# Performance work log

Measured on AMD Instinct MI355X. Metric: run time of the kernel, lower is better.

## Reference

```python
import jax, jax.numpy as jnp
import numpy as np

B, LD, LQ = 32, 512, 32
E, NF = 300, 4
D = E + NF            # doc_input_size = 304
M = 16                # fofe_max_length == max_len
ALPHA = 0.9
VOCAB = 50000
H = 256
SAMPLE_NUM = 256
POS_N = 128           # int(sample_num * (1 - neg_ratio))
NEG_N = SAMPLE_NUM - POS_N
R = min(M, LD - 2)    # candidate negative lengths = 16
PPL = NEG_N // R + 1  # negatives drawn per length = 9


def setup_inputs() -> dict:
    key = jax.random.key(0)
    ks = jax.random.split(key, 16)
    emb = jax.random.normal(ks[0], (VOCAB, E), jnp.float32) * 0.1
    emb = emb.at[0].set(0.0)  # padding_idx=0
    doc = jax.random.randint(ks[1], (B, LD), 1, VOCAB)
    doc_f = jax.random.normal(ks[2], (B, LD, NF), jnp.float32) * 0.1
    query = jax.random.randint(ks[3], (B, LQ), 1, VOCAB)
    target_s = jax.random.randint(ks[4], (B,), 1, LD - M - 2)
    span = jax.random.randint(ks[5], (B,), 0, M)  # ans_span = target_e - target_s < fofe_max_length
    target_e = target_s + span
    rand_length = jax.random.permutation(ks[6], R)  # torch.randperm(min(max_len, L-2))
    # rand_position[i] ~ randint(1, LD - rand_length[i] - 1)
    u = jax.random.uniform(ks[7], (R, PPL))
    size = (LD - rand_length - 2).astype(jnp.float32)[:, None]
    rand_position = 1 + jnp.floor(u * size).astype(jnp.int32)
    rand_idx = jax.random.randint(ks[8], (NEG_N,), 0, B)  # faithful to original (dim-0 size used as bound)
    perm_idx = jax.random.permutation(ks[9], SAMPLE_NUM)

    def w(k, o, i):
        return jax.random.normal(k, (o, i), jnp.float32) * (1.0 / np.sqrt(i))

    CIN = 3 * D + E  # 1212
    W1 = w(ks[10], 4 * H, CIN)
    W2 = w(ks[11], 4 * H, 4 * H)
    W3 = w(ks[12], 4 * H, 4 * H)
    W4 = w(ks[13], 2 * H, 4 * H)
    W5 = w(ks[14], 1, 2 * H)
    doc_mask = jnp.zeros((B, LD), bool)
    query_mask = jnp.zeros((B, LQ), bool)
    return dict(doc=doc, doc_f=doc_f, query=query, target_s=target_s, target_e=target_e,
                doc_mask=doc_mask, query_mask=query_mask, emb=emb,
                W1=W1, W2=W2, W3=W3, W4=W4, W5=W5,
                rand_length=rand_length, rand_position=rand_position,
                rand_idx=rand_idx, perm_idx=perm_idx)


def _fofe_codes(x):
    """x: [B, D, LD] -> forward/inverse FOFE codes [B, D, M, LD].
    fwd[b,c,l,t] = sum_{k=0}^{l} alpha^k x[b,c,t-k]; inv mirrors to the right."""
    fwd_terms = jnp.stack(
        [(ALPHA ** k) * jnp.pad(x, ((0, 0), (0, 0), (k, 0)))[..., :LD] for k in range(M)], axis=2)
    inv_terms = jnp.stack(
        [(ALPHA ** k) * jnp.pad(x, ((0, 0), (0, 0), (0, k)))[..., k:] for k in range(M)], axis=2)
    return jnp.cumsum(fwd_terms, axis=2), jnp.cumsum(inv_terms, axis=2)


def _cnn(x, W1, W2, W3, W4, W5):
    h = jax.nn.relu(jnp.einsum('oi,bis->bos', W1, x))
    h = jax.nn.relu(jnp.einsum('oi,bis->bos', W2, h))
    h = jax.nn.relu(jnp.einsum('oi,bis->bos', W3, h))
    h = jax.nn.relu(jnp.einsum('oi,bis->bos', W4, h))
    return jax.nn.sigmoid(jnp.einsum('oi,bis->bos', W5, h))


def reference(doc, doc_f, query, target_s, target_e, doc_mask, query_mask, emb,
              W1, W2, W3, W4, W5, rand_length, rand_position, rand_idx, perm_idx):
    # input_embedding (dropout_emb = 0, pos/ner disabled)
    doc_input = jnp.concatenate([emb[doc], doc_f], axis=-1)  # [B, LD, D]
    x = jnp.swapaxes(doc_input, 1, 2)                         # [B, D, LD]
    fwd, inv = _fofe_codes(x)                                 # [B, D, M, LD] each

    # --- positive samples: gold span + left/right full contexts ---
    b = jnp.arange(B)
    span = target_e - target_s
    ans = fwd[b, :, span, target_e]                               # [B, D]
    l_ctx = fwd[b, :, M - 1, jnp.maximum(target_s - 1, 0)]        # [B, D]
    r_ctx = inv[b, :, M - 1, jnp.minimum(target_e + 1, LD - 1)]   # [B, D]
    pos = jnp.concatenate([l_ctx, ans, r_ctx], axis=-1)          # [B, 3D]
    pos = jnp.broadcast_to(pos[:, :, None], (B, 3 * D, POS_N))

    # --- negative samples: random spans of each length in rand_length ---
    rl = rand_length[:, None]                                     # [R, 1]
    neg_ans = fwd[:, :, rl, rand_position].reshape(B, D, R * PPL)
    neg_l = fwd[:, :, M - 1, rand_position - 1].reshape(B, D, R * PPL)
    neg_r = inv[:, :, M - 1, rand_position + rl + 1].reshape(B, D, R * PPL)
    rand_cat = jnp.concatenate([neg_l, neg_ans, neg_r], axis=1)   # [B, 3D, R*PPL]
    neg = rand_cat[:, :, rand_idx]                                # [B, 3D, NEG_N]

    # --- shuffle pos+neg, build query FOFE, run cnn, mse (sum) loss ---
    ctx_ans = jnp.concatenate([pos, neg], axis=-1)[:, :, perm_idx]
    target = jnp.concatenate(
        [jnp.ones((B, 1, POS_N), jnp.float32), jnp.zeros((B, 1, NEG_N), jnp.float32)],
        axis=-1)[:, :, perm_idx]
    qw = ALPHA ** jnp.arange(LQ - 1, -1, -1, dtype=jnp.float32)   # fofe_linear weights
    qf = jnp.einsum('t,bte->be', qw, emb[query])                  # [B, E]
    qb = jnp.broadcast_to(qf[:, :, None], (B, E, SAMPLE_NUM))
    dq_input = jnp.concatenate([ctx_ans, qb], axis=1)             # [B, 3D+E, S]
    score = _cnn(dq_input, W1, W2, W3, W4, W5)                    # [B, 1, S]
    loss = jnp.sum((score - target) ** 2)                         # mse_loss(size_average=False)
    return loss
```

## Files before the change

### kernel.cpp

```cpp
#include <hip/hip_runtime.h>
#include <hip/hip_bf16.h>

#define B_    32
#define LD_   512
#define LQ_   32
#define E_    300
#define NF_   4
#define D_    304
#define M_    16
#define ALPHA_ 0.9f
#define CIN_  1212
#define KP1_  1280
#define NCOL_ 1056
#define NPAD_ 1088
#define PPL_  9
#define NEG_N_ 128

typedef short short8 __attribute__((ext_vector_type(8)));
typedef float f32x4 __attribute__((ext_vector_type(4)));

__device__ __forceinline__ unsigned short f2bf(float f) {
    unsigned int x = __float_as_uint(f);
    unsigned int r = (x + 0x7FFFu + ((x >> 16) & 1u)) >> 16;
    return (unsigned short)r;
}

__global__ __launch_bounds__(320) void prep(
    const int* __restrict__ doc, const float* __restrict__ doc_f,
    const int* __restrict__ query,
    const int* __restrict__ target_s, const int* __restrict__ target_e,
    const float* __restrict__ emb,
    const int* __restrict__ rand_length, const int* __restrict__ rand_position,
    const float* __restrict__ W1, const float* __restrict__ W2,
    const float* __restrict__ W3, const float* __restrict__ W4,
    unsigned short* __restrict__ W1b, unsigned short* __restrict__ W2b,
    unsigned short* __restrict__ W3b, unsigned short* __restrict__ W4b,
    unsigned short* __restrict__ Ft, float* __restrict__ zbuf,
    unsigned* __restrict__ done)
{
    int bid = blockIdx.x;
    int tid = threadIdx.x;

    if (bid < NCOL_) {
        int b = bid / 33;
        int col = bid % 33;
        __shared__ int   s_t[3][16];
        __shared__ float s_w[3][16];
        __shared__ int   s_row[3][16];
        if (tid < 48) {
            int part = tid >> 4, k = tid & 15;
            int t; float valid;
            if (col == 0) {
                int ts = target_s[b], te = target_e[b];
                int span = te - ts;
                if (part == 0)      { t = ts - 1 - k;  valid = (t >= 0) ? 1.f : 0.f; }
                else if (part == 1) { t = te - k;      valid = (k <= span && t >= 0) ? 1.f : 0.f; }
                else                { t = te + 1 + k;  valid = (t < LD_) ? 1.f : 0.f; }
            } else {
                int j = col - 1;
                int r = j / PPL_, p = j - r * PPL_;
                int rl = rand_length[r];
                int rp = rand_position[r * PPL_ + p];
                if (part == 0)      { t = rp - 1 - k;      valid = (t >= 0) ? 1.f : 0.f; }
                else if (part == 1) { t = rp - k;          valid = (k <= rl && t >= 0) ? 1.f : 0.f; }
                else                { t = rp + rl + 1 + k; valid = (t < LD_) ? 1.f : 0.f; }
            }
            float w = (valid != 0.f) ? powf(ALPHA_, (float)k) : 0.f;
            t = min(max(t, 0), LD_ - 1);
            s_t[part][k] = t;
            s_w[part][k] = w;
            s_row[part][k] = doc[b * LD_ + t];
        }
        __syncthreads();

        unsigned short* out = Ft + (size_t)bid * KP1_;
        int g = tid;
        if (g < 228) {
            int part = g / 76;
            int g2 = g - part * 76;
            int cc = g2 * 4;
            float ax = 0.f, ay = 0.f, az = 0.f, aw = 0.f;
            if (cc < 300) {
                for (int i = 0; i < 16; ++i) {
                    float4 v = *(const float4*)(emb + (size_t)s_row[part][i] * E_ + cc);
                    float wv = s_w[part][i];
                    ax += wv * v.x; ay += wv * v.y; az += wv * v.z; aw += wv * v.w;
                }
            } else {
                for (int i = 0; i < 16; ++i) {
                    float4 v = *(const float4*)(doc_f + ((size_t)b * LD_ + s_t[part][i]) * NF_);
                    float wv = s_w[part][i];
                    ax += wv * v.x; ay += wv * v.y; az += wv * v.z; aw += wv * v.w;
                }
            }
            ushort4 o; o.x = f2bf(ax); o.y = f2bf(ay); o.z = f2bf(az); o.w = f2bf(aw);
            *(ushort4*)(out + 4 * g) = o;
        } else if (g < 303) {
            int ce = (g - 228) * 4;
            float ax = 0.f, ay = 0.f, az = 0.f, aw = 0.f;
            float wv = powf(ALPHA_, (float)(LQ_ - 1));
            for (int i = 0; i < 32; ++i) {
                int row = query[b * LQ_ + i];
                float4 v = *(const float4*)(emb + (size_t)row * E_ + ce);
                ax += wv * v.x; ay += wv * v.y; az += wv * v.z; aw += wv * v.w;
                wv *= (1.0f / ALPHA_);
            }
            ushort4 o; o.x = f2bf(ax); o.y = f2bf(ay); o.z = f2bf(az); o.w = f2bf(aw);
            *(ushort4*)(out + 4 * g) = o;
        } else {
            ushort4 z; z.x = 0; z.y = 0; z.z = 0; z.w = 0;
            *(ushort4*)(out + 4 * g) = z;
        }
    } else if (bid < 2000) {
        const long n1 = 1024L * 320;
        const long n2 = 1024L * 1024L / 4;
        const long n4 = 512L * 1024L / 4;
        const long total = n1 + 2 * n2 + n4;
        long stride = 944L * 320L;
        for (long i = (long)(bid - NCOL_) * 320L + tid; i < total; i += stride) {
            ushort4 o;
            if (i < n1) {
                long m = i / 320; int k4 = (int)(i - m * 320);
                if (k4 < 303) {
                    float4 v = *(const float4*)(W1 + m * CIN_ + k4 * 4);
                    o.x = f2bf(v.x); o.y = f2bf(v.y); o.z = f2bf(v.z); o.w = f2bf(v.w);
                } else { o.x = 0; o.y = 0; o.z = 0; o.w = 0; }
                *(ushort4*)(W1b + i * 4) = o;
            } else if (i < n1 + n2) {
                long j = i - n1;
                float4 v = *(const float4*)(W2 + j * 4);
                o.x = f2bf(v.x); o.y = f2bf(v.y); o.z = f2bf(v.z); o.w = f2bf(v.w);
                *(ushort4*)(W2b + j * 4) = o;
            } else if (i < n1 + 2 * n2) {
                long j = i - n1 - n2;
                float4 v = *(const float4*)(W3 + j * 4);
                o.x = f2bf(v.x); o.y = f2bf(v.y); o.z = f2bf(v.z); o.w = f2bf(v.w);
                *(ushort4*)(W3b + j * 4) = o;
            } else {
                long j = i - n1 - 2 * n2;
                float4 v = *(const float4*)(W4 + j * 4);
                o.x = f2bf(v.x); o.y = f2bf(v.y); o.z = f2bf(v.z); o.w = f2bf(v.w);
                *(ushort4*)(W4b + j * 4) = o;
            }
        }
    } else if (bid < 2032) {
        int row = NCOL_ + (bid - 2000);
        ushort4 z; z.x = 0; z.y = 0; z.z = 0; z.w = 0;
        *(ushort4*)(Ft + (size_t)row * KP1_ + tid * 4) = z;
    } else {
        for (int i = tid; i < NPAD_; i += 320) zbuf[i] = 0.f;
        if (tid == 0) *done = 0u;
    }
}

struct GemmS { unsigned short A[2][64][72]; unsigned short B[2][64][72]; };

__device__ __forceinline__ void gemm_core(
    const unsigned short* __restrict__ A,
    const unsigned short* __restrict__ Bm,
    int K, int m0, int n0, GemmS& sh, f32x4 acc[4])
{
    int tid = threadIdx.x;
    int w = tid >> 6, lane = tid & 63;
    int wm = (w >> 1) * 32, wn = (w & 1) * 32;
    int lr = tid >> 2;
    int ls = (tid & 3) * 16;
    int fr = lane & 15, fk = (lane >> 4) * 8;

    const unsigned short* Arow = A + (size_t)(m0 + lr) * K + ls;
    const unsigned short* Brow = Bm + (size_t)(n0 + lr) * K + ls;

    #pragma unroll
    for (int t = 0; t < 4; ++t) { acc[t][0]=0.f; acc[t][1]=0.f; acc[t][2]=0.f; acc[t][3]=0.f; }

    int nk = K >> 6;
    *(uint4*)&sh.A[0][lr][ls]     = *(const uint4*)(Arow);
    *(uint4*)&sh.A[0][lr][ls + 8] = *(const uint4*)(Arow + 8);
    *(uint4*)&sh.B[0][lr][ls]     = *(const uint4*)(Brow);
    *(uint4*)&sh.B[0][lr][ls + 8] = *(const uint4*)(Brow + 8);
    __syncthreads();
    int cur = 0;
    for (int i = 0; i < nk; ++i) {
        uint4 na0, na1, nb0, nb1;
        bool more = (i + 1 < nk);
        if (more) {
            const unsigned short* An = Arow + (size_t)(i + 1) * 64;
            const unsigned short* Bn = Brow + (size_t)(i + 1) * 64;
            na0 = *(const uint4*)(An);
            na1 = *(const uint4*)(An + 8);
            nb0 = *(const uint4*)(Bn);
            nb1 = *(const uint4*)(Bn + 8);
        }
        #pragma unroll
        for (int s = 0; s < 2; ++s) {
            short8 fa0 = *(const short8*)&sh.A[cur][wm + fr][s * 32 + fk];
            short8 fa1 = *(const short8*)&sh.A[cur][wm + 16 + fr][s * 32 + fk];
            short8 fb0 = *(const short8*)&sh.B[cur][wn + fr][s * 32 + fk];
            short8 fb1 = *(const short8*)&sh.B[cur][wn + 16 + fr][s * 32 + fk];
            acc[0] = __builtin_amdgcn_mfma_f32_16x16x32_bf16(fa0, fb0, acc[0], 0, 0, 0);
            acc[1] = __builtin_amdgcn_mfma_f32_16x16x32_bf16(fa0, fb1, acc[1], 0, 0, 0);
            acc[2] = __builtin_amdgcn_mfma_f32_16x16x32_bf16(fa1, fb0, acc[2], 0, 0, 0);
            acc[3] = __builtin_amdgcn_mfma_f32_16x16x32_bf16(fa1, fb1, acc[3], 0, 0, 0);
        }
        if (more) {
            int nb = cur ^ 1;
            *(uint4*)&sh.A[nb][lr][ls]     = na0;
            *(uint4*)&sh.A[nb][lr][ls + 8] = na1;
            *(uint4*)&sh.B[nb][lr][ls]     = nb0;
            *(uint4*)&sh.B[nb][lr][ls + 8] = nb1;
        }
        __syncthreads();
        cur ^= 1;
    }
}

__global__ __launch_bounds__(256) void gemm_relu(
    const unsigned short* __restrict__ A,
    const unsigned short* __restrict__ Bm,
    unsigned short* __restrict__ C, int M, int K)
{
    __shared__ GemmS sh;
    int m0 = blockIdx.x * 64, n0 = blockIdx.y * 64;
    f32x4 acc[4];
    gemm_core(A, Bm, K, m0, n0, sh, acc);
    int tid = threadIdx.x;
    int w = tid >> 6, lane = tid & 63;
    int wm = (w >> 1) * 32, wn = (w & 1) * 32;
    int rbase = (lane >> 4) * 4;
    int cb = lane & 15;
    #pragma unroll
    for (int t = 0; t < 4; ++t) {
        int MT = t >> 1, NT = t & 1;
        int m = m0 + wm + MT * 16 + rbase;
        int n = n0 + wn + NT * 16 + cb;
        ushort4 o;
        o.x = f2bf(fmaxf(acc[t][0], 0.f));
        o.y = f2bf(fmaxf(acc[t][1], 0.f));
        o.z = f2bf(fmaxf(acc[t][2], 0.f));
        o.w = f2bf(fmaxf(acc[t][3], 0.f));
        *(ushort4*)(C + (size_t)n * M + m) = o;
    }
}

__global__ __launch_bounds__(256) void gemm4_score_loss(
    const unsigned short* __restrict__ A,
    const unsigned short* __restrict__ Bm,
    const float* __restrict__ W5, const int* __restrict__ rand_idx,
    float* __restrict__ zbuf, unsigned* __restrict__ done,
    float* __restrict__ out, int M, int K)
{
    __shared__ GemmS sh;
    __shared__ int s_flag;
    __shared__ int s_cnt[32];
    __shared__ float s_red[256];
    int m0 = blockIdx.x * 64, n0 = blockIdx.y * 64;
    f32x4 acc[4];
    gemm_core(A, Bm, K, m0, n0, sh, acc);
    int tid = threadIdx.x;
    int w = tid >> 6, lane = tid & 63;
    int wm = (w >> 1) * 32, wn = (w & 1) * 32;
    int fr = lane & 15, fq = lane >> 4;
    #pragma unroll
    for (int NT = 0; NT < 2; ++NT) {
        float p = 0.f;
        #pragma unroll
        for (int MT = 0; MT < 2; ++MT) {
            const f32x4 a = acc[MT * 2 + NT];
            int mb = m0 + wm + MT * 16 + fq * 4;
            p += fmaxf(a[0], 0.f) * W5[mb]
               + fmaxf(a[1], 0.f) * W5[mb + 1]
               + fmaxf(a[2], 0.f) * W5[mb + 2]
               + fmaxf(a[3], 0.f) * W5[mb + 3];
        }
        p += __shfl_down(p, 32);
        p += __shfl_down(p, 16);
        if (fq == 0) {
            int n = n0 + wn + NT * 16 + fr;
            atomicAdd(&zbuf[n], p);
        }
    }
    __syncthreads();
    if (tid == 0) {
        unsigned old = __hip_atomic_fetch_add(done, 1u, __ATOMIC_ACQ_REL,
                                              __HIP_MEMORY_SCOPE_AGENT);
        s_flag = (old == 8 * 17 - 1) ? 1 : 0;
    }
    __syncthreads();
    if (s_flag) {
        if (tid < 32) s_cnt[tid] = 0;
        __syncthreads();
        if (tid < NEG_N_) atomicAdd(&s_cnt[rand_idx[tid]], 1);
        __syncthreads();
        float accv = 0.f;
        for (int c = tid; c < NCOL_; c += 256) {
            float z = __hip_atomic_load(&zbuf[c], __ATOMIC_ACQUIRE,
                                        __HIP_MEMORY_SCOPE_AGENT);
            float s = 1.f / (1.f + expf(-z));
            int c33 = c % 33;
            if (c33 == 0) { float d = s - 1.f; accv += 128.f * d * d; }
            else          { accv += (float)s_cnt[c33 - 1] * s * s; }
        }
        s_red[tid] = accv;
        __syncthreads();
        for (int o = 128; o > 0; o >>= 1) {
            if (tid < o) s_red[tid] += s_red[tid + o];
            __syncthreads();
        }
        if (tid == 0) out[0] = s_red[0];
    }
}

extern "C" void kernel_launch(void* const* d_in, const int* in_sizes, int n_in,
                              void* d_out, int out_size, void* d_ws, size_t ws_size,
                              hipStream_t stream)
{
    const int*   doc        = (const int*)d_in[0];
    const float* doc_f      = (const float*)d_in[1];
    const int*   query      = (const int*)d_in[2];
    const int*   target_s   = (const int*)d_in[3];
    const int*   target_e   = (const int*)d_in[4];
    const float* emb        = (const float*)d_in[7];
    const float* W1         = (const float*)d_in[8];
    const float* W2         = (const float*)d_in[9];
    const float* W3         = (const float*)d_in[10];
    const float* W4         = (const float*)d_in[11];
    const float* W5         = (const float*)d_in[12];
    const int*   rand_length   = (const int*)d_in[13];
    const int*   rand_position = (const int*)d_in[14];
    const int*   rand_idx      = (const int*)d_in[15];

    char* ws = (char*)d_ws;
    size_t off = 0;
    auto alloc = [&](size_t bytes) {
        void* p = ws + off;
        off = (off + bytes + 255) & ~(size_t)255;
        return p;
    };
    unsigned short* W1b = (unsigned short*)alloc((size_t)1024 * KP1_ * 2);
    unsigned short* W2b = (unsigned short*)alloc((size_t)1024 * 1024 * 2);
    unsigned short* W3b = (unsigned short*)alloc((size_t)1024 * 1024 * 2);
    unsigned short* W4b = (unsigned short*)alloc((size_t)512 * 1024 * 2);
    unsigned short* Ft  = (unsigned short*)alloc((size_t)NPAD_ * KP1_ * 2);
    unsigned short* hA  = (unsigned short*)alloc((size_t)NPAD_ * 1024 * 2);
    unsigned short* hB  = (unsigned short*)alloc((size_t)NPAD_ * 1024 * 2);
    float*    zbuf      = (float*)alloc((size_t)NPAD_ * sizeof(float));
    unsigned* done      = (unsigned*)alloc(256);
    (void)ws_size; (void)in_sizes; (void)n_in; (void)out_size;

    prep<<<dim3(2033), dim3(320), 0, stream>>>(
        doc, doc_f, query, target_s, target_e, emb,
        rand_length, rand_position,
        W1, W2, W3, W4, W1b, W2b, W3b, W4b, Ft, zbuf, done);

    gemm_relu<<<dim3(16, 17), dim3(256), 0, stream>>>(W1b, Ft, hA, 1024, KP1_);
    gemm_relu<<<dim3(16, 17), dim3(256), 0, stream>>>(W2b, hA, hB, 1024, 1024);
    gemm_relu<<<dim3(16, 17), dim3(256), 0, stream>>>(W3b, hB, hA, 1024, 1024);
    gemm4_score_loss<<<dim3(8, 17), dim3(256), 0, stream>>>(
        W4b, hA, W5, rand_idx, zbuf, done, (float*)d_out, 512, 1024);
}
```

Baseline: 190.0 us.

## Halve GEMM M-tile to double block count and add two-stage register prefetch

Shrinks the GEMM tile from 64x64 to 32x64 so each layer launches twice as many workgroups (544 instead of 272, 272 instead of 136 for the last layer), giving better coverage of the many CUs on the device. The main loop is restructured into an unrolled two-buffer scheme that keeps two K-slices of prefetched global loads in registers, and launch bounds request two blocks per CU. The smaller tile lowers arithmetic intensity and increases redundant B-operand reads. The completion counter threshold is updated to match the new grid.

```diff
diff --git a/kernel.cpp b/kernel.cpp
--- a/kernel.cpp
+++ b/kernel.cpp
@@ -153,96 +153,111 @@
     }
 }
 
-struct GemmS { unsigned short A[2][64][72]; unsigned short B[2][64][72]; };
+struct GemmS { unsigned short A[2][32][72]; unsigned short B[2][64][72]; };
 
 __device__ __forceinline__ void gemm_core(
     const unsigned short* __restrict__ A,
     const unsigned short* __restrict__ Bm,
-    int K, int m0, int n0, GemmS& sh, f32x4 acc[4])
+    int K, int m0, int n0, GemmS& sh, f32x4 acc[2])
 {
     int tid = threadIdx.x;
     int w = tid >> 6, lane = tid & 63;
-    int wm = (w >> 1) * 32, wn = (w & 1) * 32;
-    int lr = tid >> 2;
-    int ls = (tid & 3) * 16;
+    int wm = (w >> 1) * 16, wn = (w & 1) * 32;
+    int lr = tid >> 3;
+    int ls = (tid & 7) * 8;
     int fr = lane & 15, fk = (lane >> 4) * 8;
 
-    const unsigned short* Arow = A + (size_t)(m0 + lr) * K + ls;
-    const unsigned short* Brow = Bm + (size_t)(n0 + lr) * K + ls;
-
-    #pragma unroll
-    for (int t = 0; t < 4; ++t) { acc[t][0]=0.f; acc[t][1]=0.f; acc[t][2]=0.f; acc[t][3]=0.f; }
+    const unsigned short* Ar  = A  + (size_t)(m0 + lr) * K + ls;
+    const unsigned short* Br0 = Bm + (size_t)(n0 + lr) * K + ls;
+    const unsigned short* Br1 = Bm + (size_t)(n0 + lr + 32) * K + ls;
+
+    acc[0][0]=0.f; acc[0][1]=0.f; acc[0][2]=0.f; acc[0][3]=0.f;
+    acc[1][0]=0.f; acc[1][1]=0.f; acc[1][2]=0.f; acc[1][3]=0.f;
 
     int nk = K >> 6;
-    *(uint4*)&sh.A[0][lr][ls]     = *(const uint4*)(Arow);
-    *(uint4*)&sh.A[0][lr][ls + 8] = *(const uint4*)(Arow + 8);
-    *(uint4*)&sh.B[0][lr][ls]     = *(const uint4*)(Brow);
-    *(uint4*)&sh.B[0][lr][ls + 8] = *(const uint4*)(Brow + 8);
+
+    uint4 ra0, rb00, rb10;
+    uint4 ra1, rb01, rb11;
+
+    ra0 = *(const uint4*)(Ar);        rb00 = *(const uint4*)(Br0);        rb10 = *(const uint4*)(Br1);
+    ra1 = *(const uint4*)(Ar + 64);   rb01 = *(const uint4*)(Br0 + 64);   rb11 = *(const uint4*)(Br1 + 64);
+    *(uint4*)&sh.A[0][lr][ls]      = ra0;
+    *(uint4*)&sh.B[0][lr][ls]      = rb00;
+    *(uint4*)&sh.B[0][lr + 32][ls] = rb10;
+    ra0 = *(const uint4*)(Ar + 128);  rb00 = *(const uint4*)(Br0 + 128);  rb10 = *(const uint4*)(Br1 + 128);
     __syncthreads();
-    int cur = 0;
-    for (int i = 0; i < nk; ++i) {
-        uint4 na0, na1, nb0, nb1;
-        bool more = (i + 1 < nk);
-        if (more) {
-            const unsigned short* An = Arow + (size_t)(i + 1) * 64;
-            const unsigned short* Bn = Brow + (size_t)(i + 1) * 64;
-            na0 = *(const uint4*)(An);
-            na1 = *(const uint4*)(An + 8);
-            nb0 = *(const uint4*)(Bn);
-            nb1 = *(const uint4*)(Bn + 8);
-        }
+
+    for (int i = 0; i < nk; i += 2) {
         #pragma unroll
         for (int s = 0; s < 2; ++s) {
-            short8 fa0 = *(const short8*)&sh.A[cur][wm + fr][s * 32 + fk];
-            short8 fa1 = *(const short8*)&sh.A[cur][wm + 16 + fr][s * 32 + fk];
-            short8 fb0 = *(const short8*)&sh.B[cur][wn + fr][s * 32 + fk];
-            short8 fb1 = *(const short8*)&sh.B[cur][wn + 16 + fr][s * 32 + fk];
-            acc[0] = __builtin_amdgcn_mfma_f32_16x16x32_bf16(fa0, fb0, acc[0], 0, 0, 0);
-            acc[1] = __builtin_amdgcn_mfma_f32_16x16x32_bf16(fa0, fb1, acc[1], 0, 0, 0);
-            acc[2] = __builtin_amdgcn_mfma_f32_16x16x32_bf16(fa1, fb0, acc[2], 0, 0, 0);
-            acc[3] = __builtin_amdgcn_mfma_f32_16x16x32_bf16(fa1, fb1, acc[3], 0, 0, 0);
-        }
-        if (more) {
-            int nb = cur ^ 1;
-            *(uint4*)&sh.A[nb][lr][ls]     = na0;
-            *(uint4*)&sh.A[nb][lr][ls + 8] = na1;
-            *(uint4*)&sh.B[nb][lr][ls]     = nb0;
-            *(uint4*)&sh.B[nb][lr][ls + 8] = nb1;
-        }
-        __syncthreads();
-        cur ^= 1;
-    }
-}
-
-__global__ __launch_bounds__(256) void gemm_relu(
+            short8 fa  = *(const short8*)&sh.A[0][wm + fr][s * 32 + fk];
+            short8 fb0 = *(const short8*)&sh.B[0][wn + fr][s * 32 + fk];
+            short8 fb1 = *(const short8*)&sh.B[0][wn + 16 + fr][s * 32 + fk];
+            acc[0] = __builtin_amdgcn_mfma_f32_16x16x32_bf16(fa, fb0, acc[0], 0, 0, 0);
+            acc[1] = __builtin_amdgcn_mfma_f32_16x16x32_bf16(fa, fb1, acc[1], 0, 0, 0);
+        }
+        *(uint4*)&sh.A[1][lr][ls]      = ra1;
+        *(uint4*)&sh.B[1][lr][ls]      = rb01;
+        *(uint4*)&sh.B[1][lr + 32][ls] = rb11;
+        if (i + 3 < nk) {
+            const unsigned short* An  = Ar  + (size_t)(i + 3) * 64;
+            const unsigned short* Bn0 = Br0 + (size_t)(i + 3) * 64;
+            const unsigned short* Bn1 = Br1 + (size_t)(i + 3) * 64;
+            ra1 = *(const uint4*)(An); rb01 = *(const uint4*)(Bn0); rb11 = *(const uint4*)(Bn1);
+        }
+        __syncthreads();
+
+        #pragma unroll
+        for (int s = 0; s < 2; ++s) {
+            short8 fa  = *(const short8*)&sh.A[1][wm + fr][s * 32 + fk];
+            short8 fb0 = *(const short8*)&sh.B[1][wn + fr][s * 32 + fk];
+            short8 fb1 = *(const short8*)&sh.B[1][wn + 16 + fr][s * 32 + fk];
+            acc[0] = __builtin_amdgcn_mfma_f32_16x16x32_bf16(fa, fb0, acc[0], 0, 0, 0);
+            acc[1] = __builtin_amdgcn_mfma_f32_16x16x32_bf16(fa, fb1, acc[1], 0, 0, 0);
+        }
+        if (i + 2 < nk) {
+            *(uint4*)&sh.A[0][lr][ls]      = ra0;
+            *(uint4*)&sh.B[0][lr][ls]      = rb00;
+            *(uint4*)&sh.B[0][lr + 32][ls] = rb10;
+            if (i + 4 < nk) {
+                const unsigned short* An  = Ar  + (size_t)(i + 4) * 64;
+                const unsigned short* Bn0 = Br0 + (size_t)(i + 4) * 64;
+                const unsigned short* Bn1 = Br1 + (size_t)(i + 4) * 64;
+                ra0 = *(const uint4*)(An); rb00 = *(const uint4*)(Bn0); rb10 = *(const uint4*)(Bn1);
+            }
+            __syncthreads();
+        }
+    }
+}
+
+__global__ __launch_bounds__(256, 2) void gemm_relu(
     const unsigned short* __restrict__ A,
     const unsigned short* __restrict__ Bm,
     unsigned short* __restrict__ C, int M, int K)
 {
     __shared__ GemmS sh;
-    int m0 = blockIdx.x * 64, n0 = blockIdx.y * 64;
-    f32x4 acc[4];
+    int m0 = blockIdx.x * 32, n0 = blockIdx.y * 64;
+    f32x4 acc[2];
     gemm_core(A, Bm, K, m0, n0, sh, acc);
     int tid = threadIdx.x;
     int w = tid >> 6, lane = tid & 63;
-    int wm = (w >> 1) * 32, wn = (w & 1) * 32;
+    int wm = (w >> 1) * 16, wn = (w & 1) * 32;
     int rbase = (lane >> 4) * 4;
     int cb = lane & 15;
     #pragma unroll
-    for (int t = 0; t < 4; ++t) {
-        int MT = t >> 1, NT = t & 1;
-        int m = m0 + wm + MT * 16 + rbase;
+    for (int NT = 0; NT < 2; ++NT) {
+        int m = m0 + wm + rbase;
         int n = n0 + wn + NT * 16 + cb;
         ushort4 o;
-        o.x = f2bf(fmaxf(acc[t][0], 0.f));
-        o.y = f2bf(fmaxf(acc[t][1], 0.f));
-        o.z = f2bf(fmaxf(acc[t][2], 0.f));
-        o.w = f2bf(fmaxf(acc[t][3], 0.f));
+        o.x = f2bf(fmaxf(acc[NT][0], 0.f));
+        o.y = f2bf(fmaxf(acc[NT][1], 0.f));
+        o.z = f2bf(fmaxf(acc[NT][2], 0.f));
+        o.w = f2bf(fmaxf(acc[NT][3], 0.f));
         *(ushort4*)(C + (size_t)n * M + m) = o;
     }
 }
 
-__global__ __launch_bounds__(256) void gemm4_score_loss(
+__global__ __launch_bounds__(256, 2) void gemm4_score_loss(
     const unsigned short* __restrict__ A,
     const unsigned short* __restrict__ Bm,
     const float* __restrict__ W5, const int* __restrict__ rand_idx,
@@ -253,25 +268,21 @@
     __shared__ int s_flag;
     __shared__ int s_cnt[32];
     __shared__ float s_red[256];
-    int m0 = blockIdx.x * 64, n0 = blockIdx.y * 64;
-    f32x4 acc[4];
+    int m0 = blockIdx.x * 32, n0 = blockIdx.y * 64;
+    f32x4 acc[2];
     gemm_core(A, Bm, K, m0, n0, sh, acc);
     int tid = threadIdx.x;
     int w = tid >> 6, lane = tid & 63;
-    int wm = (w >> 1) * 32, wn = (w & 1) * 32;
+    int wm = (w >> 1) * 16, wn = (w & 1) * 32;
     int fr = lane & 15, fq = lane >> 4;
     #pragma unroll
     for (int NT = 0; NT < 2; ++NT) {
-        float p = 0.f;
-        #pragma unroll
-        for (int MT = 0; MT < 2; ++MT) {
-            const f32x4 a = acc[MT * 2 + NT];
-            int mb = m0 + wm + MT * 16 + fq * 4;
-            p += fmaxf(a[0], 0.f) * W5[mb]
-               + fmaxf(a[1], 0.f) * W5[mb + 1]
-               + fmaxf(a[2], 0.f) * W5[mb + 2]
-               + fmaxf(a[3], 0.f) * W5[mb + 3];
-        }
+        const f32x4 a = acc[NT];
+        int mb = m0 + wm + fq * 4;
+        float p = fmaxf(a[0], 0.f) * W5[mb]
+                + fmaxf(a[1], 0.f) * W5[mb + 1]
+                + fmaxf(a[2], 0.f) * W5[mb + 2]
+                + fmaxf(a[3], 0.f) * W5[mb + 3];
         p += __shfl_down(p, 32);
         p += __shfl_down(p, 16);
         if (fq == 0) {
@@ -283,7 +294,7 @@
     if (tid == 0) {
         unsigned old = __hip_atomic_fetch_add(done, 1u, __ATOMIC_ACQ_REL,
                                               __HIP_MEMORY_SCOPE_AGENT);
-        s_flag = (old == 8 * 17 - 1) ? 1 : 0;
+        s_flag = (old == 16 * 17 - 1) ? 1 : 0;
     }
     __syncthreads();
     if (s_flag) {
@@ -352,9 +363,9 @@
         rand_length, rand_position,
         W1, W2, W3, W4, W1b, W2b, W3b, W4b, Ft, zbuf, done);
 
-    gemm_relu<<<dim3(16, 17), dim3(256), 0, stream>>>(W1b, Ft, hA, 1024, KP1_);
-    gemm_relu<<<dim3(16, 17), dim3(256), 0, stream>>>(W2b, hA, hB, 1024, 1024);
-    gemm_relu<<<dim3(16, 17), dim3(256), 0, stream>>>(W3b, hB, hA, 1024, 1024);
-    gemm4_score_loss<<<dim3(8, 17), dim3(256), 0, stream>>>(
+    gemm_relu<<<dim3(32, 17), dim3(256), 0, stream>>>(W1b, Ft, hA, 1024, KP1_);
+    gemm_relu<<<dim3(32, 17), dim3(256), 0, stream>>>(W2b, hA, hB, 1024, 1024);
+    gemm_relu<<<dim3(32, 17), dim3(256), 0, stream>>>(W3b, hB, hA, 1024, 1024);
+    gemm4_score_loss<<<dim3(16, 17), dim3(256), 0, stream>>>(
         W4b, hA, W5, rand_idx, zbuf, done, (float*)d_out, 512, 1024);
 }
```

Result: no change. 189.5 us (-0.3%).

## Fuse four GEMM launches into one persistent kernel with grid barriers

Applied to the files above, without the earlier changes.

Replaces the three gemm_relu launches and the final score/loss launch with a single 512-block kernel. Each layer's tiles are computed by the first 272 (or 136) blocks, and a software grid barrier built on atomics separates the layers. This removes kernel launch gaps and tail effects between layers. The cost is spin-wait barrier overhead, idle blocks in every phase, and a deadlock risk if all 512 blocks cannot be co-resident.

```diff
diff --git a/kernel.cpp b/kernel.cpp
--- a/kernel.cpp
+++ b/kernel.cpp
@@ -15,6 +15,7 @@
 #define NPAD_ 1088
 #define PPL_  9
 #define NEG_N_ 128
+#define GRID_FUSED_ 512
 
 typedef short short8 __attribute__((ext_vector_type(8)));
 typedef float f32x4 __attribute__((ext_vector_type(4)));
@@ -149,7 +150,7 @@
         *(ushort4*)(Ft + (size_t)row * KP1_ + tid * 4) = z;
     } else {
         for (int i = tid; i < NPAD_; i += 320) zbuf[i] = 0.f;
-        if (tid == 0) *done = 0u;
+        if (tid < 8) done[tid] = 0u;
     }
 }
 
@@ -214,13 +215,11 @@
     }
 }
 
-__global__ __launch_bounds__(256) void gemm_relu(
+__device__ __forceinline__ void gemm_tile_relu(
     const unsigned short* __restrict__ A,
     const unsigned short* __restrict__ Bm,
-    unsigned short* __restrict__ C, int M, int K)
-{
-    __shared__ GemmS sh;
-    int m0 = blockIdx.x * 64, n0 = blockIdx.y * 64;
+    unsigned short* __restrict__ C, int M, int K, int m0, int n0, GemmS& sh)
+{
     f32x4 acc[4];
     gemm_core(A, Bm, K, m0, n0, sh, acc);
     int tid = threadIdx.x;
@@ -242,51 +241,84 @@
     }
 }
 
-__global__ __launch_bounds__(256) void gemm4_score_loss(
-    const unsigned short* __restrict__ A,
-    const unsigned short* __restrict__ Bm,
-    const float* __restrict__ W5, const int* __restrict__ rand_idx,
-    float* __restrict__ zbuf, unsigned* __restrict__ done,
-    float* __restrict__ out, int M, int K)
+__device__ __forceinline__ void gsync(unsigned* __restrict__ sync, unsigned nblk)
+{
+    __syncthreads();
+    if (threadIdx.x == 0) {
+        unsigned gen = __hip_atomic_load(&sync[1], __ATOMIC_ACQUIRE,
+                                         __HIP_MEMORY_SCOPE_SYSTEM);
+        unsigned old = __hip_atomic_fetch_add(&sync[0], 1u, __ATOMIC_ACQ_REL,
+                                              __HIP_MEMORY_SCOPE_SYSTEM);
+        if (old == nblk - 1u) {
+            __hip_atomic_store(&sync[0], 0u, __ATOMIC_RELAXED,
+                               __HIP_MEMORY_SCOPE_SYSTEM);
+            __hip_atomic_fetch_add(&sync[1], 1u, __ATOMIC_ACQ_REL,
+                                   __HIP_MEMORY_SCOPE_SYSTEM);
+        } else {
+            while (__hip_atomic_load(&sync[1], __ATOMIC_ACQUIRE,
+                                     __HIP_MEMORY_SCOPE_SYSTEM) == gen)
+                __builtin_amdgcn_s_sleep(2);
+        }
+    }
+    __syncthreads();
+}
+
+__global__ __launch_bounds__(256, 2) void gemm_fused(
+    const unsigned short* __restrict__ W1b, const unsigned short* __restrict__ W2b,
+    const unsigned short* __restrict__ W3b, const unsigned short* __restrict__ W4b,
+    const unsigned short* __restrict__ Ft, unsigned short* __restrict__ hA,
+    unsigned short* __restrict__ hB, const float* __restrict__ W5,
+    const int* __restrict__ rand_idx, float* __restrict__ zbuf,
+    unsigned* __restrict__ sync, float* __restrict__ out)
 {
     __shared__ GemmS sh;
-    __shared__ int s_flag;
     __shared__ int s_cnt[32];
     __shared__ float s_red[256];
-    int m0 = blockIdx.x * 64, n0 = blockIdx.y * 64;
-    f32x4 acc[4];
-    gemm_core(A, Bm, K, m0, n0, sh, acc);
+    int bid = blockIdx.x;
     int tid = threadIdx.x;
-    int w = tid >> 6, lane = tid & 63;
-    int wm = (w >> 1) * 32, wn = (w & 1) * 32;
-    int fr = lane & 15, fq = lane >> 4;
-    #pragma unroll
-    for (int NT = 0; NT < 2; ++NT) {
-        float p = 0.f;
+
+    if (bid < 272)
+        gemm_tile_relu(W1b, Ft, hA, 1024, KP1_, (bid & 15) * 64, (bid >> 4) * 64, sh);
+    gsync(sync, GRID_FUSED_);
+
+    if (bid < 272)
+        gemm_tile_relu(W2b, hA, hB, 1024, 1024, (bid & 15) * 64, (bid >> 4) * 64, sh);
+    gsync(sync, GRID_FUSED_);
+
+    if (bid < 272)
+        gemm_tile_relu(W3b, hB, hA, 1024, 1024, (bid & 15) * 64, (bid >> 4) * 64, sh);
+    gsync(sync, GRID_FUSED_);
+
+    if (bid < 136) {
+        int m0 = (bid & 7) * 64, n0 = (bid >> 3) * 64;
+        f32x4 acc[4];
+        gemm_core(W4b, hA, 1024, m0, n0, sh, acc);
+        int w = tid >> 6, lane = tid & 63;
+        int wm = (w >> 1) * 32, wn = (w & 1) * 32;
+        int fr = lane & 15, fq = lane >> 4;
         #pragma unroll
-        for (int MT = 0; MT < 2; ++MT) {
-            const f32x4 a = acc[MT * 2 + NT];
-            int mb = m0 + wm + MT * 16 + fq * 4;
-            p += fmaxf(a[0], 0.f) * W5[mb]
-               + fmaxf(a[1], 0.f) * W5[mb + 1]
-               + fmaxf(a[2], 0.f) * W5[mb + 2]
-               + fmaxf(a[3], 0.f) * W5[mb + 3];
-        }
-        p += __shfl_down(p, 32);
-        p += __shfl_down(p, 16);
-        if (fq == 0) {
-            int n = n0 + wn + NT * 16 + fr;
-            atomicAdd(&zbuf[n], p);
-        }
-    }
-    __syncthreads();
-    if (tid == 0) {
-        unsigned old = __hip_atomic_fetch_add(done, 1u, __ATOMIC_ACQ_REL,
-                                              __HIP_MEMORY_SCOPE_AGENT);
-        s_flag = (old == 8 * 17 - 1) ? 1 : 0;
-    }
-    __syncthreads();
-    if (s_flag) {
+        for (int NT = 0; NT < 2; ++NT) {
+            float p = 0.f;
+            #pragma unroll
+            for (int MT = 0; MT < 2; ++MT) {
+                const f32x4 a = acc[MT * 2 + NT];
+                int mb = m0 + wm + MT * 16 + fq * 4;
+                p += fmaxf(a[0], 0.f) * W5[mb]
+                   + fmaxf(a[1], 0.f) * W5[mb + 1]
+                   + fmaxf(a[2], 0.f) * W5[mb + 2]
+                   + fmaxf(a[3], 0.f) * W5[mb + 3];
+            }
+            p += __shfl_down(p, 32);
+            p += __shfl_down(p, 16);
+            if (fq == 0) {
+                int n = n0 + wn + NT * 16 + fr;
+                atomicAdd(&zbuf[n], p);
+            }
+        }
+    }
+    gsync(sync, GRID_FUSED_);
+
+    if (bid == 0) {
         if (tid < 32) s_cnt[tid] = 0;
         __syncthreads();
         if (tid < NEG_N_) atomicAdd(&s_cnt[rand_idx[tid]], 1);
@@ -352,9 +384,7 @@
         rand_length, rand_position,
         W1, W2, W3, W4, W1b, W2b, W3b, W4b, Ft, zbuf, done);
 
-    gemm_relu<<<dim3(16, 17), dim3(256), 0, stream>>>(W1b, Ft, hA, 1024, KP1_);
-    gemm_relu<<<dim3(16, 17), dim3(256), 0, stream>>>(W2b, hA, hB, 1024, 1024);
-    gemm_relu<<<dim3(16, 17), dim3(256), 0, stream>>>(W3b, hB, hA, 1024, 1024);
-    gemm4_score_loss<<<dim3(8, 17), dim3(256), 0, stream>>>(
-        W4b, hA, W5, rand_idx, zbuf, done, (float*)d_out, 512, 1024);
-}
+    gemm_fused<<<dim3(GRID_FUSED_), dim3(256), 0, stream>>>(
+        W1b, W2b, W3b, W4b, Ft, hA, hB, W5, rand_idx, zbuf, done,
+        (float*)d_out);
+}
```

Measured after the change: 522.6 us. 2.75x slower.

## Stage per-batch document embeddings in LDS for FOFE feature building

Applied to the files above, without the earlier changes.

Restructures the prep feature stage so each block owns one batch and a 60-channel slice, loading the full 512-row document embedding slice and query rows into shared memory once. All 33 columns (positive plus negatives) and three parts are then computed from LDS instead of issuing 16 scattered global gathers per column. This cuts redundant embedding reads but uses roughly 134KB of LDS per block with only 160 blocks, so occupancy and parallelism drop and the whole 512-row slice is loaded even though only windows are needed. The weight-conversion blocks keep the same stride, so their work distribution is unchanged.

```diff
diff --git a/kernel.cpp b/kernel.cpp
--- a/kernel.cpp
+++ b/kernel.cpp
@@ -41,83 +41,91 @@
     int bid = blockIdx.x;
     int tid = threadIdx.x;
 
-    if (bid < NCOL_) {
-        int b = bid / 33;
-        int col = bid % 33;
-        __shared__ int   s_t[3][16];
-        __shared__ float s_w[3][16];
-        __shared__ int   s_row[3][16];
-        if (tid < 48) {
-            int part = tid >> 4, k = tid & 15;
-            int t; float valid;
-            if (col == 0) {
+    if (bid < 160) {
+        int b = bid / 5, slice = bid % 5;
+        int ch0 = slice * 60;
+        __shared__ float Ds[512][60];
+        __shared__ float Fs[512][4];
+        __shared__ float Qs[32][60];
+        __shared__ int   s_doc[512];
+        __shared__ float s_aw[16];
+        __shared__ float s_qw[32];
+
+        for (int r = tid; r < LD_; r += 320) s_doc[r] = doc[b * LD_ + r];
+        if (tid < 16) s_aw[tid] = powf(ALPHA_, (float)tid);
+        else if (tid < 48) s_qw[tid - 16] = powf(ALPHA_, (float)(LQ_ - 1 - (tid - 16)));
+        __syncthreads();
+
+        for (int idx = tid; idx < 512 * 15; idx += 320) {
+            int r = idx / 15, f = idx - r * 15;
+            *(float4*)&Ds[r][f * 4] =
+                *(const float4*)(emb + (size_t)s_doc[r] * E_ + ch0 + f * 4);
+        }
+        for (int idx = tid; idx < 32 * 15; idx += 320) {
+            int r = idx / 15, f = idx - r * 15;
+            *(float4*)&Qs[r][f * 4] =
+                *(const float4*)(emb + (size_t)query[b * LQ_ + r] * E_ + ch0 + f * 4);
+        }
+        if (slice == 4) {
+            for (int r = tid; r < LD_; r += 320)
+                *(float4*)&Fs[r][0] = *(const float4*)(doc_f + ((size_t)b * LD_ + r) * NF_);
+        }
+        __syncthreads();
+
+        int c = tid & 63;
+        int slot = tid >> 6;
+        for (int jp = slot; jp < 99; jp += 5) {
+            int j = jp / 3, part = jp - j * 3;
+            int A, kl;
+            if (j == 0) {
                 int ts = target_s[b], te = target_e[b];
-                int span = te - ts;
-                if (part == 0)      { t = ts - 1 - k;  valid = (t >= 0) ? 1.f : 0.f; }
-                else if (part == 1) { t = te - k;      valid = (k <= span && t >= 0) ? 1.f : 0.f; }
-                else                { t = te + 1 + k;  valid = (t < LD_) ? 1.f : 0.f; }
+                A = (part == 0) ? ts : te;
+                kl = te - ts;
             } else {
-                int j = col - 1;
-                int r = j / PPL_, p = j - r * PPL_;
-                int rl = rand_length[r];
-                int rp = rand_position[r * PPL_ + p];
-                if (part == 0)      { t = rp - 1 - k;      valid = (t >= 0) ? 1.f : 0.f; }
-                else if (part == 1) { t = rp - k;          valid = (k <= rl && t >= 0) ? 1.f : 0.f; }
-                else                { t = rp + rl + 1 + k; valid = (t < LD_) ? 1.f : 0.f; }
-            }
-            float w = (valid != 0.f) ? powf(ALPHA_, (float)k) : 0.f;
-            t = min(max(t, 0), LD_ - 1);
-            s_t[part][k] = t;
-            s_w[part][k] = w;
-            s_row[part][k] = doc[b * LD_ + t];
-        }
-        __syncthreads();
-
-        unsigned short* out = Ft + (size_t)bid * KP1_;
-        int g = tid;
-        if (g < 228) {
-            int part = g / 76;
-            int g2 = g - part * 76;
-            int cc = g2 * 4;
-            float ax = 0.f, ay = 0.f, az = 0.f, aw = 0.f;
-            if (cc < 300) {
-                for (int i = 0; i < 16; ++i) {
-                    float4 v = *(const float4*)(emb + (size_t)s_row[part][i] * E_ + cc);
-                    float wv = s_w[part][i];
-                    ax += wv * v.x; ay += wv * v.y; az += wv * v.z; aw += wv * v.w;
-                }
-            } else {
-                for (int i = 0; i < 16; ++i) {
-                    float4 v = *(const float4*)(doc_f + ((size_t)b * LD_ + s_t[part][i]) * NF_);
-                    float wv = s_w[part][i];
-                    ax += wv * v.x; ay += wv * v.y; az += wv * v.z; aw += wv * v.w;
-                }
-            }
-            ushort4 o; o.x = f2bf(ax); o.y = f2bf(ay); o.z = f2bf(az); o.w = f2bf(aw);
-            *(ushort4*)(out + 4 * g) = o;
-        } else if (g < 303) {
-            int ce = (g - 228) * 4;
-            float ax = 0.f, ay = 0.f, az = 0.f, aw = 0.f;
-            float wv = powf(ALPHA_, (float)(LQ_ - 1));
-            for (int i = 0; i < 32; ++i) {
-                int row = query[b * LQ_ + i];
-                float4 v = *(const float4*)(emb + (size_t)row * E_ + ce);
-                ax += wv * v.x; ay += wv * v.y; az += wv * v.z; aw += wv * v.w;
-                wv *= (1.0f / ALPHA_);
-            }
-            ushort4 o; o.x = f2bf(ax); o.y = f2bf(ay); o.z = f2bf(az); o.w = f2bf(aw);
-            *(ushort4*)(out + 4 * g) = o;
-        } else {
-            ushort4 z; z.x = 0; z.y = 0; z.z = 0; z.w = 0;
-            *(ushort4*)(out + 4 * g) = z;
-        }
-    } else if (bid < 2000) {
+                int jj = j - 1, r = jj / PPL_, p = jj - r * PPL_;
+                int rl = rand_length[r], rp = rand_position[r * PPL_ + p];
+                A = (part == 2) ? (rp + rl) : rp;
+                kl = rl;
+            }
+            float acc = 0.f;
+            #pragma unroll
+            for (int k = 0; k < 16; ++k) {
+                int t; float valid;
+                if (part == 0)      { t = A - 1 - k; valid = (t >= 0) ? 1.f : 0.f; }
+                else if (part == 1) { t = A - k;     valid = (k <= kl && t >= 0) ? 1.f : 0.f; }
+                else                { t = A + 1 + k; valid = (t < LD_) ? 1.f : 0.f; }
+                t = min(max(t, 0), LD_ - 1);
+                float w = valid * s_aw[k];
+                float v = (c < 60) ? Ds[t][c] : Fs[t][c & 3];
+                acc += w * v;
+            }
+            if (c < 60 || slice == 4) {
+                int ch = (c < 60) ? (ch0 + c) : (300 + (c - 60));
+                Ft[(size_t)(b * 33 + j) * KP1_ + part * 304 + ch] = f2bf(acc);
+            }
+        }
+
+        if (tid < 60) {
+            float qa = 0.f;
+            for (int i = 0; i < 32; ++i) qa += s_qw[i] * Qs[i][tid];
+            unsigned short qb = f2bf(qa);
+            for (int j = 0; j < 33; ++j)
+                Ft[(size_t)(b * 33 + j) * KP1_ + 912 + ch0 + tid] = qb;
+        }
+
+        if (slice == 0) {
+            for (int idx = tid; idx < 33 * 34; idx += 320) {
+                int j = idx / 34, u = idx - j * 34;
+                *(unsigned int*)(Ft + (size_t)(b * 33 + j) * KP1_ + 1212 + u * 2) = 0u;
+            }
+        }
+    } else if (bid < 1104) {
         const long n1 = 1024L * 320;
         const long n2 = 1024L * 1024L / 4;
         const long n4 = 512L * 1024L / 4;
         const long total = n1 + 2 * n2 + n4;
         long stride = 944L * 320L;
-        for (long i = (long)(bid - NCOL_) * 320L + tid; i < total; i += stride) {
+        for (long i = (long)(bid - 160) * 320L + tid; i < total; i += stride) {
             ushort4 o;
             if (i < n1) {
                 long m = i / 320; int k4 = (int)(i - m * 320);
@@ -143,13 +151,13 @@
                 *(ushort4*)(W4b + j * 4) = o;
             }
         }
-    } else if (bid < 2032) {
-        int row = NCOL_ + (bid - 2000);
+    } else if (bid < 1136) {
+        int row = NCOL_ + (bid - 1104);
         ushort4 z; z.x = 0; z.y = 0; z.z = 0; z.w = 0;
         *(ushort4*)(Ft + (size_t)row * KP1_ + tid * 4) = z;
     } else {
         for (int i = tid; i < NPAD_; i += 320) zbuf[i] = 0.f;
-        if (tid == 0) *done = 0u;
+        if (tid < 8) done[tid] = 0u;
     }
 }
 
@@ -347,7 +355,7 @@
     unsigned* done      = (unsigned*)alloc(256);
     (void)ws_size; (void)in_sizes; (void)n_in; (void)out_size;
 
-    prep<<<dim3(2033), dim3(320), 0, stream>>>(
+    prep<<<dim3(1137), dim3(320), 0, stream>>>(
         doc, doc_f, query, target_s, target_e, emb,
         rand_length, rand_position,
         W1, W2, W3, W4, W1b, W2b, W3b, W4b, Ft, zbuf, done);
```

New measurement: 236.9 us. 24.7% more time.
